# Performance work log

Hardware: AMD Instinct MI355X
Metric: run time of the kernel (lower is better)

## Reference

```python
import jax, jax.numpy as jnp
import numpy as np

NUM_HEADS = 8
MODEL_DIM = 512
HIDDEN_DIM = 64  # model_dim // num_heads
BATCH = 4
SEQ = 1024


def setup_inputs() -> dict:
    key = jax.random.key(0)
    kx, kq, kk, kv, ko = jax.random.split(key, 5)
    # xavier_uniform bound for [model_dim, hidden_dim] fan pair
    bqkv = float(np.sqrt(6.0 / (MODEL_DIM + HIDDEN_DIM)))
    bo = float(np.sqrt(6.0 / (MODEL_DIM + MODEL_DIM)))
    return {
        "X": jax.random.normal(kx, (BATCH, SEQ, MODEL_DIM), dtype=jnp.float32),
        "mask": jnp.zeros((SEQ, SEQ), dtype=bool),  # unused by module
        "Wq": jax.random.uniform(kq, (NUM_HEADS, MODEL_DIM, HIDDEN_DIM), minval=-bqkv, maxval=bqkv, dtype=jnp.float32),
        "Wk": jax.random.uniform(kk, (NUM_HEADS, MODEL_DIM, HIDDEN_DIM), minval=-bqkv, maxval=bqkv, dtype=jnp.float32),
        "Wv": jax.random.uniform(kv, (NUM_HEADS, MODEL_DIM, HIDDEN_DIM), minval=-bqkv, maxval=bqkv, dtype=jnp.float32),
        "Wo": jax.random.uniform(ko, (MODEL_DIM, MODEL_DIM), minval=-bo, maxval=bo, dtype=jnp.float32),
    }


def reference(X, mask, Wq, Wk, Wv, Wo):
    # Per-head projections (replaces the replicated-tensor lin_proj with one einsum)
    q = jnp.einsum("bsm,hmd->hbsd", X, Wq)  # [h,b,s,d]
    k = jnp.einsum("bsm,hmd->hbsd", X, Wk)
    v = jnp.einsum("bsm,hmd->hbsd", X, Wv)
    # Katharopoulos feature map on q and k
    q = jax.nn.elu(q) + 1.0
    k = jax.nn.elu(k) + 1.0
    # Cumulative outer-product state S_t = sum_{i<=t} k_i v_i^T  -> [h,b,s,d,d]
    S = jnp.cumsum(k[..., :, None] * v[..., None, :], axis=2)
    V_bar = jnp.einsum("hbsd,hbsde->hbse", q, S)  # numerator
    Z = jnp.einsum("hbsd,hbsd->hbs", q, jnp.cumsum(k, axis=2))  # normalizer
    out_heads = V_bar / Z[..., None]  # [h,b,s,d]
    # combine_heads: permute to [b,s,h,d], flatten heads, project by Wo
    b, s = out_heads.shape[1], out_heads.shape[2]
    combined = jnp.transpose(out_heads, (1, 2, 0, 3)).reshape(b, s, -1)
    return jnp.einsum("bsm,mn->bsn", combined, Wo)
```

## Files before the change

### kernel.cpp

```cpp
#include <hip/hip_runtime.h>
#include <math.h>

namespace {
typedef unsigned short u16;
typedef __attribute__((ext_vector_type(8))) short bf16x8;
typedef __attribute__((ext_vector_type(4))) float f32x4;

constexpr int H  = 8;
constexpr int B  = 4;
constexpr int S  = 1024;
constexpr int M  = 512;
constexpr int D  = 64;
constexpr int BS = B * S;
constexpr int NC = 16;
constexpr int CH = 64;
constexpr int QSZ = H * B * S * D;
constexpr int NQKV = 3 * M;

__device__ __forceinline__ float elu1(float x) {
  return x > 0.f ? x + 1.f : __expf(x);
}

__device__ __forceinline__ u16 f2bf(float f) {
  unsigned u = __builtin_bit_cast(unsigned, f);
  u += 0x7fffu + ((u >> 16) & 1u);
  return (u16)(u >> 16);
}

__device__ __forceinline__ float bf2f(u16 v) {
  return __builtin_bit_cast(float, ((unsigned)v) << 16);
}

__device__ __forceinline__ void gload16(const u16* g, u16* l) {
  __builtin_amdgcn_global_load_lds(
      (const __attribute__((address_space(1))) unsigned int*)g,
      (__attribute__((address_space(3))) unsigned int*)l, 16, 0, 0);
}

__global__ __launch_bounds__(256) void prep(
    const float* __restrict__ X, const float* __restrict__ Wq,
    const float* __restrict__ Wk, const float* __restrict__ Wv,
    const float* __restrict__ Wo, u16* __restrict__ Xb,
    u16* __restrict__ WCT, u16* __restrict__ WoT) {
  __shared__ float t[64][65];
  const int bid = blockIdx.x;
  if (bid < 2048) {
    const int i = bid * 256 + threadIdx.x;
    const float4 v = reinterpret_cast<const float4*>(X)[i];
    u16 o[4] = {f2bf(v.x), f2bf(v.y), f2bf(v.z), f2bf(v.w)};
    *reinterpret_cast<uint2*>(Xb + i * 4) = *reinterpret_cast<uint2*>(o);
  } else if (bid < 2240) {
    const int bb = bid - 2048;
    const int mt = bb & 7, ph = bb >> 3;
    const int p = ph >> 3, h = ph & 7;
    const float* W = ((p == 0) ? Wq : (p == 1) ? Wk : Wv) + h * (M * D);
    const int m0 = mt * 64;
#pragma unroll
    for (int j = 0; j < 4; ++j) {
      const int i = j * 256 + threadIdx.x;
      const int mm = i >> 4, dd = (i & 15) * 4;
      const float4 v = *reinterpret_cast<const float4*>(W + (m0 + mm) * D + dd);
      t[mm][dd + 0] = v.x; t[mm][dd + 1] = v.y;
      t[mm][dd + 2] = v.z; t[mm][dd + 3] = v.w;
    }
    __syncthreads();
    const int dd = threadIdx.x >> 2, qr = (threadIdx.x & 3) * 16;
    u16* o = WCT + (p * M + h * D + dd) * M + m0 + qr;
#pragma unroll
    for (int i = 0; i < 16; ++i) o[i] = f2bf(t[qr + i][dd]);
  } else {
    const int bb = bid - 2240;
    const int m0 = (bb & 7) * 64, n0 = (bb >> 3) * 64;
#pragma unroll
    for (int j = 0; j < 4; ++j) {
      const int i = j * 256 + threadIdx.x;
      const int mm = i >> 4, nn = (i & 15) * 4;
      const float4 v = *reinterpret_cast<const float4*>(Wo + (m0 + mm) * M + n0 + nn);
      t[mm][nn + 0] = v.x; t[mm][nn + 1] = v.y;
      t[mm][nn + 2] = v.z; t[mm][nn + 3] = v.w;
    }
    __syncthreads();
    const int nn = threadIdx.x >> 2, qr = (threadIdx.x & 3) * 16;
    u16* o = WoT + (n0 + nn) * M + m0 + qr;
#pragma unroll
    for (int i = 0; i < 16; ++i) o[i] = f2bf(t[qr + i][nn]);
  }
}

__global__ __launch_bounds__(512) void gemm_qkv(const u16* __restrict__ A,
                                                const u16* __restrict__ BT,
                                                u16* __restrict__ qb,
                                                u16* __restrict__ kb,
                                                u16* __restrict__ kTb,
                                                u16* __restrict__ vTb) {
  __shared__ alignas(16) u16 As[2][4096];
  __shared__ alignas(16) u16 Bs[2][4096];
  const int tid = threadIdx.x;
  const int wave = tid >> 6, lane = tid & 63;
  const int r0 = blockIdx.x * 128, c0 = blockIdx.y * 128;
  const int wr = (wave >> 1) * 32, wc = (wave & 1) * 64;
  const int l15 = lane & 15, lk = lane >> 4;

  f32x4 acc[2][4] = {};
  const u16* gA = A + (size_t)(r0 + wave * 16 + (lane >> 2)) * 512 + (lane & 3) * 8;
  const u16* gB = BT + (size_t)(c0 + wave * 16 + (lane >> 2)) * 512 + (lane & 3) * 8;

#define STG_QKV(kt, b)                          \
  {                                             \
    const int ko = (kt) * 32;                   \
    gload16(gA + ko, &As[b][wave * 512]);       \
    gload16(gB + ko, &Bs[b][wave * 512]);       \
  }

  STG_QKV(0, 0);
  __syncthreads();
  for (int kt = 0; kt < 16; ++kt) {
    if (kt < 15) STG_QKV(kt + 1, (kt + 1) & 1);
    const bf16x8* As8 = reinterpret_cast<const bf16x8*>(As[kt & 1]);
    const bf16x8* Bs8 = reinterpret_cast<const bf16x8*>(Bs[kt & 1]);
    bf16x8 af[2], bff[4];
#pragma unroll
    for (int mf = 0; mf < 2; ++mf)
      af[mf] = As8[(wr + mf * 16 + l15) * 4 + lk];
#pragma unroll
    for (int nf = 0; nf < 4; ++nf)
      bff[nf] = Bs8[(wc + nf * 16 + l15) * 4 + lk];
#pragma unroll
    for (int mf = 0; mf < 2; ++mf)
#pragma unroll
      for (int nf = 0; nf < 4; ++nf)
        acc[mf][nf] = __builtin_amdgcn_mfma_f32_16x16x32_bf16(
            af[mf], bff[nf], acc[mf][nf], 0, 0, 0);
    __syncthreads();
  }
#undef STG_QKV

#pragma unroll
  for (int nf = 0; nf < 4; ++nf) {
    const int col = c0 + wc + nf * 16 + l15;
    const int p = col >> 9, hh = (col >> 6) & 7, dd = col & 63;
#pragma unroll
    for (int mf = 0; mf < 2; ++mf) {
      const int rowb = r0 + wr + mf * 16 + lk * 4;
      const int b = rowb >> 10, s = rowb & 1023;
      const int hb = hh * B + b;
      u16 ov[4];
#pragma unroll
      for (int r = 0; r < 4; ++r) {
        float v = acc[mf][nf][r];
        if (p < 2) v = elu1(v);
        ov[r] = f2bf(v);
      }
      if (p == 0) {
#pragma unroll
        for (int r = 0; r < 4; ++r)
          qb[((size_t)(hb << 10) + s + r) * 64 + dd] = ov[r];
      } else if (p == 1) {
#pragma unroll
        for (int r = 0; r < 4; ++r)
          kb[((size_t)(hb << 10) + s + r) * 64 + dd] = ov[r];
        *reinterpret_cast<uint2*>(kTb + ((size_t)(hb * 64 + dd) << 10) + s) =
            *reinterpret_cast<uint2*>(ov);
      } else {
        *reinterpret_cast<uint2*>(vTb + ((size_t)(hb * 64 + dd) << 10) + s) =
            *reinterpret_cast<uint2*>(ov);
      }
    }
  }
}

__global__ __launch_bounds__(512) void gemm_out(const u16* __restrict__ A,
                                                const u16* __restrict__ BT,
                                                float* __restrict__ out) {
  __shared__ alignas(16) u16 As[2][4096];
  __shared__ alignas(16) u16 Bs[2][2048];
  const int tid = threadIdx.x;
  const int wave = tid >> 6, lane = tid & 63;
  const int r0 = blockIdx.x * 128, c0 = blockIdx.y * 64;
  const int wr = (wave >> 1) * 32, wc = (wave & 1) * 32;
  const int l15 = lane & 15, lk = lane >> 4;

  f32x4 acc[2][2] = {};
  const u16* gA = A + (size_t)(r0 + wave * 16 + (lane >> 2)) * 512 + (lane & 3) * 8;
  const u16* gB = BT + (size_t)(c0 + (wave - 4) * 16 + (lane >> 2)) * 512 + (lane & 3) * 8;

#define STG_OUT(kt, b)                                        \
  {                                                           \
    const int ko = (kt) * 32;                                 \
    gload16(gA + ko, &As[b][wave * 512]);                     \
    if (wave >= 4) gload16(gB + ko, &Bs[b][(wave - 4) * 512]); \
  }

  STG_OUT(0, 0);
  __syncthreads();
  for (int kt = 0; kt < 16; ++kt) {
    if (kt < 15) STG_OUT(kt + 1, (kt + 1) & 1);
    const bf16x8* As8 = reinterpret_cast<const bf16x8*>(As[kt & 1]);
    const bf16x8* Bs8 = reinterpret_cast<const bf16x8*>(Bs[kt & 1]);
    bf16x8 a[2], b[2];
#pragma unroll
    for (int mf = 0; mf < 2; ++mf)
      a[mf] = As8[(wr + mf * 16 + l15) * 4 + lk];
#pragma unroll
    for (int nf = 0; nf < 2; ++nf)
      b[nf] = Bs8[(wc + nf * 16 + l15) * 4 + lk];
#pragma unroll
    for (int mf = 0; mf < 2; ++mf)
#pragma unroll
      for (int nf = 0; nf < 2; ++nf)
        acc[mf][nf] = __builtin_amdgcn_mfma_f32_16x16x32_bf16(
            a[mf], b[nf], acc[mf][nf], 0, 0, 0);
    __syncthreads();
  }
#undef STG_OUT

#pragma unroll
  for (int nf = 0; nf < 2; ++nf) {
    const int col = c0 + wc + nf * 16 + l15;
#pragma unroll
    for (int mf = 0; mf < 2; ++mf)
#pragma unroll
      for (int r = 0; r < 4; ++r) {
        const int row = r0 + wr + mf * 16 + lk * 4 + r;
        out[(size_t)row * M + col] = acc[mf][nf][r];
      }
  }
}

__global__ __launch_bounds__(256) void chunkstate_mfma(
    const u16* __restrict__ kTb, const u16* __restrict__ vTb,
    float* __restrict__ G32, float* __restrict__ Ks) {
  const int tid = threadIdx.x, wave = tid >> 6, lane = tid & 63;
  const int bx = blockIdx.x, hb = bx >> 4, cc = bx & 15, s0 = cc * CH;
  const u16* vbase = vTb + ((size_t)hb * 64) * 1024 + s0;
  const u16* kbase = kTb + ((size_t)hb * 64) * 1024 + s0;

  bf16x8 av[2];
#pragma unroll
  for (int ks = 0; ks < 2; ++ks)
    av[ks] = *reinterpret_cast<const bf16x8*>(
        vbase + (size_t)(wave * 16 + (lane & 15)) * 1024 + ks * 32 + (lane >> 4) * 8);

  f32x4 acc[4] = {};
#pragma unroll
  for (int fd = 0; fd < 4; ++fd)
#pragma unroll
    for (int ks = 0; ks < 2; ++ks) {
      bf16x8 bk = *reinterpret_cast<const bf16x8*>(
          kbase + (size_t)(fd * 16 + (lane & 15)) * 1024 + ks * 32 + (lane >> 4) * 8);
      acc[fd] = __builtin_amdgcn_mfma_f32_16x16x32_bf16(av[ks], bk, acc[fd], 0, 0, 0);
    }

  float* Gp = G32 + (size_t)bx * 4096;
#pragma unroll
  for (int fd = 0; fd < 4; ++fd)
#pragma unroll
    for (int r = 0; r < 4; ++r) {
      const int e = wave * 16 + (lane >> 4) * 4 + r;
      const int d = fd * 16 + (lane & 15);
      Gp[e * 64 + d] = acc[fd][r];
    }

  const int d = tid >> 2, tq = tid & 3;
  const u16* kp = kbase + (size_t)d * 1024 + tq * 16;
  float ks = 0.f;
#pragma unroll
  for (int j = 0; j < 16; ++j) ks += bf2f(kp[j]);
  ks += __shfl_xor(ks, 1);
  ks += __shfl_xor(ks, 2);
  if (tq == 0) Ks[bx * 64 + d] = ks;
}

__global__ __launch_bounds__(256) void prefix_kernel(
    const float* __restrict__ G32, u16* __restrict__ GTb,
    float* __restrict__ Ks) {
  const int hb = blockIdx.x, eg = blockIdx.y;
  const int tid = threadIdx.x;
  const int e = eg * 4 + (tid >> 6), d = tid & 63;
  const size_t base = ((size_t)(hb * 16) * 64 + e) * 64 + d;
  float acc = 0.f;
#pragma unroll
  for (int c = 0; c < 16; ++c) {
    const float v = G32[base + (size_t)c * 4096];
    GTb[base + (size_t)c * 4096] = f2bf(acc);
    acc += v;
  }
  if (eg == 0 && tid < 64) {
    float ka = 0.f;
#pragma unroll
    for (int c = 0; c < 16; ++c) {
      const int idx = (hb * 16 + c) * 64 + tid;
      const float v = Ks[idx];
      Ks[idx] = ka;
      ka += v;
    }
  }
}

__global__ __launch_bounds__(256) void chunkout_mfma(
    const u16* __restrict__ qb, const u16* __restrict__ kb,
    const u16* __restrict__ vTb, const u16* __restrict__ GTb,
    const float* __restrict__ Kc, u16* __restrict__ att) {
  __shared__ alignas(16) u16 Qs[4096], Kls[4096], Vs[4096], Gs[4096], Astg[4096];
  const int tid = threadIdx.x, wave = tid >> 6, lane = tid & 63;
  const int bx = blockIdx.x, hb = bx >> 4, cc = bx & 15, s0 = cc * CH;
  const int h = hb >> 2, b = hb & 3;

  {
    const u16* qg = qb + ((size_t)(hb << 10) + s0) * 64;
    const u16* kg = kb + ((size_t)(hb << 10) + s0) * 64;
    const u16* gg = GTb + (size_t)bx * 4096;
#pragma unroll
    for (int j = 0; j < 2; ++j) {
      const int off = j * 2048 + wave * 512;
      gload16(qg + off + lane * 8, Qs + off);
      gload16(kg + off + lane * 8, Kls + off);
      gload16(gg + off + lane * 8, Gs + off);
    }
    const u16* vg = vTb + ((size_t)hb * 64) * 1024 + s0;
#pragma unroll
    for (int j = 0; j < 2; ++j) {
      const int e0 = j * 32 + wave * 8;
      gload16(vg + (size_t)(e0 + (lane >> 3)) * 1024 + (lane & 7) * 8,
              Vs + e0 * 64);
    }
  }
  __syncthreads();

  const bf16x8* Qs8 = reinterpret_cast<const bf16x8*>(Qs);
  const bf16x8* Ks8 = reinterpret_cast<const bf16x8*>(Kls);
  const bf16x8* Vs8 = reinterpret_cast<const bf16x8*>(Vs);
  const bf16x8* Gs8 = reinterpret_cast<const bf16x8*>(Gs);
  const bf16x8* As8 = reinterpret_cast<const bf16x8*>(Astg);

  const int i0 = wave * 16;
  const int l15 = lane & 15, lk = lane >> 4;

  bf16x8 aq[2];
#pragma unroll
  for (int ks = 0; ks < 2; ++ks)
    aq[ks] = Qs8[(i0 + l15) * 8 + ks * 4 + lk];

  f32x4 a[4] = {};
#pragma unroll
  for (int fj = 0; fj < 4; ++fj)
#pragma unroll
    for (int ks = 0; ks < 2; ++ks) {
      bf16x8 bk = Ks8[(fj * 16 + l15) * 8 + ks * 4 + lk];
      a[fj] = __builtin_amdgcn_mfma_f32_16x16x32_bf16(aq[ks], bk, a[fj], 0, 0, 0);
    }

  const float4 kc4 = *reinterpret_cast<const float4*>(Kc + bx * 64 + l15 * 4);
  float z[4];
  const int rbase = lk * 4;
#pragma unroll
  for (int r = 0; r < 4; ++r) {
    const int il = rbase + r;
    float sum = 0.f;
#pragma unroll
    for (int fj = 0; fj < 4; ++fj) {
      const int j = fj * 16 + l15;
      if (j > i0 + il) a[fj][r] = 0.f;
      sum += a[fj][r];
    }
    const uint2 qrow = *reinterpret_cast<const uint2*>(Qs + (i0 + il) * 64 + l15 * 4);
    const u16* qr16 = reinterpret_cast<const u16*>(&qrow);
    sum += bf2f(qr16[0]) * kc4.x + bf2f(qr16[1]) * kc4.y +
           bf2f(qr16[2]) * kc4.z + bf2f(qr16[3]) * kc4.w;
    z[r] = sum;
  }
#pragma unroll
  for (int off = 1; off <= 8; off <<= 1)
#pragma unroll
    for (int r = 0; r < 4; ++r) z[r] += __shfl_xor(z[r], off);

#pragma unroll
  for (int fj = 0; fj < 4; ++fj)
#pragma unroll
    for (int r = 0; r < 4; ++r)
      Astg[(i0 + rbase + r) * 64 + fj * 16 + l15] = f2bf(a[fj][r]);

  f32x4 o[4] = {};
#pragma unroll
  for (int fe = 0; fe < 4; ++fe) {
#pragma unroll
    for (int ks = 0; ks < 2; ++ks) {
      bf16x8 bg = Gs8[(fe * 16 + l15) * 8 + ks * 4 + lk];
      o[fe] = __builtin_amdgcn_mfma_f32_16x16x32_bf16(aq[ks], bg, o[fe], 0, 0, 0);
    }
#pragma unroll
    for (int ks = 0; ks < 2; ++ks) {
      bf16x8 aa = As8[(i0 + l15) * 8 + ks * 4 + lk];
      bf16x8 bv = Vs8[(fe * 16 + l15) * 8 + ks * 4 + lk];
      o[fe] = __builtin_amdgcn_mfma_f32_16x16x32_bf16(aa, bv, o[fe], 0, 0, 0);
    }
  }

  float rz[4];
#pragma unroll
  for (int r = 0; r < 4; ++r) rz[r] = 1.f / z[r];
#pragma unroll
  for (int fe = 0; fe < 4; ++fe)
#pragma unroll
    for (int r = 0; r < 4; ++r) {
      const int srow = s0 + i0 + rbase + r;
      att[((size_t)(b << 10) + srow) * 512 + h * 64 + fe * 16 + l15] =
          f2bf(o[fe][r] * rz[r]);
    }
}

}

extern "C" void kernel_launch(void* const* d_in, const int* in_sizes, int n_in,
                              void* d_out, int out_size, void* d_ws,
                              size_t ws_size, hipStream_t stream) {
  const float* X  = (const float*)d_in[0];
  const float* Wq = (const float*)d_in[2];
  const float* Wk = (const float*)d_in[3];
  const float* Wv = (const float*)d_in[4];
  const float* Wo = (const float*)d_in[5];
  float* out = (float*)d_out;

  u16* Xb  = (u16*)d_ws;
  u16* att = Xb;
  u16* WCT = Xb + QSZ;
  u16* WoT = WCT + NQKV * M;
  u16* qb  = WoT + M * M;
  u16* kb  = qb + QSZ;
  u16* kTb = kb + QSZ;
  u16* vTb = kTb + QSZ;
  u16* GTb = vTb + QSZ;
  float* G32 = (float*)(GTb + QSZ);
  float* Ks  = G32 + QSZ;

  prep<<<dim3(2304), 256, 0, stream>>>(X, Wq, Wk, Wv, Wo, Xb, WCT, WoT);
  gemm_qkv<<<dim3(BS / 128, NQKV / 128), 512, 0, stream>>>(Xb, WCT, qb, kb,
                                                           kTb, vTb);
  chunkstate_mfma<<<dim3(H * B * NC), 256, 0, stream>>>(kTb, vTb, G32, Ks);
  prefix_kernel<<<dim3(H * B, 16), 256, 0, stream>>>(G32, GTb, Ks);
  chunkout_mfma<<<dim3(H * B * NC), 256, 0, stream>>>(qb, kb, vTb, GTb, Ks,
                                                      att);
  gemm_out<<<dim3(BS / 128, M / 64), 512, 0, stream>>>(att, WoT, out);
}
```

Before: 52.12 us.

## Fuse chunk-state GEMM and prefix scan into one per-head-batch kernel

Merges the per-chunk K^T V state computation and the cross-chunk exclusive prefix sum into a single kernel, with one block per (head, batch) holding all chunk states in shared memory. This removes a kernel launch and the fp32 global round trip of the intermediate chunk states. In exchange the grid shrinks to 32 blocks with large LDS usage, reducing parallelism. Chunk states are rounded to bf16 before being summed, which adds rounding error to the prefix.

```diff
diff --git a/kernel.cpp b/kernel.cpp
--- a/kernel.cpp
+++ b/kernel.cpp
@@ -227,72 +227,76 @@
   }
 }
 
-__global__ __launch_bounds__(256) void chunkstate_mfma(
+__global__ __launch_bounds__(256) void stateprefix(
     const u16* __restrict__ kTb, const u16* __restrict__ vTb,
-    float* __restrict__ G32, float* __restrict__ Ks) {
+    u16* __restrict__ GTb, float* __restrict__ Ks) {
+  __shared__ u16 Gl[NC * 4096];
+  __shared__ float Kss[NC * 64];
   const int tid = threadIdx.x, wave = tid >> 6, lane = tid & 63;
-  const int bx = blockIdx.x, hb = bx >> 4, cc = bx & 15, s0 = cc * CH;
-  const u16* vbase = vTb + ((size_t)hb * 64) * 1024 + s0;
-  const u16* kbase = kTb + ((size_t)hb * 64) * 1024 + s0;
-
-  bf16x8 av[2];
-#pragma unroll
-  for (int ks = 0; ks < 2; ++ks)
-    av[ks] = *reinterpret_cast<const bf16x8*>(
-        vbase + (size_t)(wave * 16 + (lane & 15)) * 1024 + ks * 32 + (lane >> 4) * 8);
-
-  f32x4 acc[4] = {};
-#pragma unroll
-  for (int fd = 0; fd < 4; ++fd)
-#pragma unroll
-    for (int ks = 0; ks < 2; ++ks) {
-      bf16x8 bk = *reinterpret_cast<const bf16x8*>(
-          kbase + (size_t)(fd * 16 + (lane & 15)) * 1024 + ks * 32 + (lane >> 4) * 8);
-      acc[fd] = __builtin_amdgcn_mfma_f32_16x16x32_bf16(av[ks], bk, acc[fd], 0, 0, 0);
-    }
-
-  float* Gp = G32 + (size_t)bx * 4096;
-#pragma unroll
-  for (int fd = 0; fd < 4; ++fd)
-#pragma unroll
-    for (int r = 0; r < 4; ++r) {
-      const int e = wave * 16 + (lane >> 4) * 4 + r;
-      const int d = fd * 16 + (lane & 15);
-      Gp[e * 64 + d] = acc[fd][r];
-    }
-
-  const int d = tid >> 2, tq = tid & 3;
-  const u16* kp = kbase + (size_t)d * 1024 + tq * 16;
-  float ks = 0.f;
-#pragma unroll
-  for (int j = 0; j < 16; ++j) ks += bf2f(kp[j]);
-  ks += __shfl_xor(ks, 1);
-  ks += __shfl_xor(ks, 2);
-  if (tq == 0) Ks[bx * 64 + d] = ks;
-}
-
-__global__ __launch_bounds__(256) void prefix_kernel(
-    const float* __restrict__ G32, u16* __restrict__ GTb,
-    float* __restrict__ Ks) {
-  const int hb = blockIdx.x, eg = blockIdx.y;
-  const int tid = threadIdx.x;
-  const int e = eg * 4 + (tid >> 6), d = tid & 63;
-  const size_t base = ((size_t)(hb * 16) * 64 + e) * 64 + d;
-  float acc = 0.f;
-#pragma unroll
-  for (int c = 0; c < 16; ++c) {
-    const float v = G32[base + (size_t)c * 4096];
-    GTb[base + (size_t)c * 4096] = f2bf(acc);
-    acc += v;
-  }
-  if (eg == 0 && tid < 64) {
+  const int hb = blockIdx.x;
+  const int l15 = lane & 15, lk = lane >> 4;
+  const u16* vbase = vTb + ((size_t)hb * 64) * 1024;
+  const u16* kbase = kTb + ((size_t)hb * 64) * 1024;
+
+  for (int i = 0; i < 4; ++i) {
+    const int c = wave * 4 + i, s0 = c * 64;
+    bf16x8 bk[4][2];
+#pragma unroll
+    for (int fd = 0; fd < 4; ++fd)
+#pragma unroll
+      for (int ks = 0; ks < 2; ++ks)
+        bk[fd][ks] = *reinterpret_cast<const bf16x8*>(
+            kbase + (size_t)(fd * 16 + l15) * 1024 + s0 + ks * 32 + lk * 8);
+#pragma unroll
+    for (int eg = 0; eg < 4; ++eg) {
+      bf16x8 av[2];
+#pragma unroll
+      for (int ks = 0; ks < 2; ++ks)
+        av[ks] = *reinterpret_cast<const bf16x8*>(
+            vbase + (size_t)(eg * 16 + l15) * 1024 + s0 + ks * 32 + lk * 8);
+      f32x4 acc[4] = {};
+#pragma unroll
+      for (int fd = 0; fd < 4; ++fd)
+#pragma unroll
+        for (int ks = 0; ks < 2; ++ks)
+          acc[fd] = __builtin_amdgcn_mfma_f32_16x16x32_bf16(av[ks], bk[fd][ks],
+                                                           acc[fd], 0, 0, 0);
+#pragma unroll
+      for (int fd = 0; fd < 4; ++fd)
+#pragma unroll
+        for (int r = 0; r < 4; ++r)
+          Gl[c * 4096 + (eg * 16 + lk * 4 + r) * 64 + fd * 16 + l15] =
+              f2bf(acc[fd][r]);
+    }
+    float ksum = 0.f;
+#pragma unroll
+    for (int j = 0; j < 8; ++j) {
+      const bf16x8 kv = *reinterpret_cast<const bf16x8*>(
+          kbase + (size_t)lane * 1024 + s0 + j * 8);
+#pragma unroll
+      for (int e = 0; e < 8; ++e) ksum += bf2f((u16)kv[e]);
+    }
+    Kss[c * 64 + lane] = ksum;
+  }
+  __syncthreads();
+
+#pragma unroll
+  for (int j = 0; j < 16; ++j) {
+    const int pos = j * 256 + tid;
+    float facc = 0.f;
+#pragma unroll
+    for (int c = 0; c < NC; ++c) {
+      const float v = bf2f(Gl[c * 4096 + pos]);
+      GTb[((size_t)(hb * NC) + c) * 4096 + pos] = f2bf(facc);
+      facc += v;
+    }
+  }
+  if (tid < 64) {
     float ka = 0.f;
 #pragma unroll
-    for (int c = 0; c < 16; ++c) {
-      const int idx = (hb * 16 + c) * 64 + tid;
-      const float v = Ks[idx];
-      Ks[idx] = ka;
-      ka += v;
+    for (int c = 0; c < NC; ++c) {
+      Ks[(hb * NC + c) * 64 + tid] = ka;
+      ka += Kss[c * 64 + tid];
     }
   }
 }
@@ -430,14 +434,12 @@
   u16* kTb = kb + QSZ;
   u16* vTb = kTb + QSZ;
   u16* GTb = vTb + QSZ;
-  float* G32 = (float*)(GTb + QSZ);
-  float* Ks  = G32 + QSZ;
+  float* Ks = (float*)(GTb + QSZ);
 
   prep<<<dim3(2304), 256, 0, stream>>>(X, Wq, Wk, Wv, Wo, Xb, WCT, WoT);
   gemm_qkv<<<dim3(BS / 128, NQKV / 128), 512, 0, stream>>>(Xb, WCT, qb, kb,
                                                            kTb, vTb);
-  chunkstate_mfma<<<dim3(H * B * NC), 256, 0, stream>>>(kTb, vTb, G32, Ks);
-  prefix_kernel<<<dim3(H * B, 16), 256, 0, stream>>>(G32, GTb, Ks);
+  stateprefix<<<dim3(H * B), 256, 0, stream>>>(kTb, vTb, GTb, Ks);
   chunkout_mfma<<<dim3(H * B * NC), 256, 0, stream>>>(qb, kb, vTb, GTb, Ks,
                                                       att);
   gemm_out<<<dim3(BS / 128, M / 64), 512, 0, stream>>>(att, WoT, out);
```

After: 63.98 us. 22.7% more time.
